# Performance work log

Measured on AMD Instinct MI355X. Metric: run time of the kernel, lower is better.

The kernel has to match this reference:

```python
import jax, jax.numpy as jnp
import numpy as np

INPUT_SIZE = 500
SENTENCE_SIZE = 128


def setup_inputs() -> dict:
    key = jax.random.key(0)
    ks = jax.random.split(key, 20)
    B, D = 16, 512
    Ho, Hi, Hu = 4, 4, 4
    dh_ori = D // Ho          # 128
    dh = D // (Hi + Hu)       # 64
    s = 0.05
    code = jax.random.normal(ks[0], (B, INPUT_SIZE, D), jnp.float32)
    # binary sentence-membership mask (which code tokens belong to each sentence)
    input_sentence = (jax.random.uniform(ks[1], (B, SENTENCE_SIZE, INPUT_SIZE)) < 0.2).astype(jnp.float32)

    def W(k, h, dout):
        return jax.random.normal(k, (h, D, dout), jnp.float32) * s

    def b(k, h, dout):
        return jax.random.normal(k, (h, dout), jnp.float32) * 0.01

    return dict(
        code=code, input_sentence=input_sentence,
        Wq_ori=W(ks[2], Ho, dh_ori), bq_ori=b(ks[3], Ho, dh_ori),
        Wk_ori=W(ks[4], Ho, dh_ori), bk_ori=b(ks[5], Ho, dh_ori),
        Wq_in=W(ks[6], Hi, dh), bq_in=b(ks[7], Hi, dh),
        Wk_in=W(ks[8], Hi, dh), bk_in=b(ks[9], Hi, dh),
        Wv_in=W(ks[10], Hi, dh), bv_in=b(ks[11], Hi, dh),
        Wq_out=W(ks[12], Hu, dh), bq_out=b(ks[13], Hu, dh),
        Wk_out=W(ks[14], Hu, dh), bk_out=b(ks[15], Hu, dh),
        Wv_out=W(ks[16], Hu, dh), bv_out=b(ks[17], Hu, dh),
    )


def _proj(x, W, b):
    # x: (B, N, D), W: (H, D, F), b: (H, F) -> (B, H, N, F), relu Dense per head
    return jax.nn.relu(jnp.einsum('bnd,hdf->bhnf', x, W) + b[:, None, :])


def reference(code, input_sentence,
              Wq_ori, bq_ori, Wk_ori, bk_ori,
              Wq_in, bq_in, Wk_in, bk_in, Wv_in, bv_in,
              Wq_out, bq_out, Wk_out, bk_out, Wv_out, bv_out):
    B, S = input_sentence.shape[0], input_sentence.shape[1]
    sent = input_sentence

    # ---- original (ori) branch: max over heads of raw QK^T, mask, matmul code ----
    q = _proj(code, Wq_ori, bq_ori)
    k = _proj(code, Wk_ori, bk_ori)
    scores_ori = jnp.einsum('bhnf,bhmf->bhnm', q, k).max(axis=1)      # (B, N, N)
    sA = jnp.einsum('bsn,bnm->bsm', sent, scores_ori)                 # (B, S, N)
    out_ori = jnp.einsum('bsm,bmd->bsd', sent * sA, code)             # (B, S, D)

    # ---- in-mask heads ----
    qi = _proj(code, Wq_in, bq_in)
    ki = _proj(code, Wk_in, bk_in)
    vi = _proj(code, Wv_in, bv_in)
    sc = jnp.einsum('bhnf,bhmf->bhnm', qi, ki)                        # (B, Hi, N, N)
    sAi = jnp.einsum('bsn,bhnm->bhsm', sent, sc)                      # (B, Hi, S, N)
    out_in = jnp.einsum('bhsm,bhmf->bhsf', sent[:, None] * sAi, vi)   # (B, Hi, S, F)

    # ---- out-mask heads ----
    qo = _proj(code, Wq_out, bq_out)
    ko = _proj(code, Wk_out, bk_out)
    vo = _proj(code, Wv_out, bv_out)
    sco = jnp.einsum('bhnf,bhmf->bhnm', qo, ko)
    sAo = jnp.einsum('bsn,bhnm->bhsm', sent, sco)
    masked = (sent - 1.0)[:, None] * sAo                              # (B, Hu, S, N)
    include = sent.sum(axis=2)[:, None, :, None]                      # (B, 1, S, 1)
    masked = masked / (INPUT_SIZE - include) * include
    out_out = jnp.einsum('bhsm,bhmf->bhsf', masked, vo)               # (B, Hu, S, F)

    # original returns a list [ori, in_0..in_Hi-1, out_0..out_Hu-1]; concat along features
    in_flat = jnp.transpose(out_in, (0, 2, 1, 3)).reshape(B, S, -1)
    out_flat = jnp.transpose(out_out, (0, 2, 1, 3)).reshape(B, S, -1)
    return jnp.concatenate([out_ori, in_flat, out_flat], axis=-1)
```

## Files before the change

kernel.cpp:

```cpp
#include <hip/hip_runtime.h>
#include <cfloat>

#define B_  16
#define N_  500
#define NP  512
#define S_  128
#define D_  512
#define FO  128
#define FI  64

typedef unsigned short u16;
typedef __attribute__((ext_vector_type(8))) short bf8;
typedef __attribute__((ext_vector_type(4))) float f4;

#define MFMA(a,b,c) __builtin_amdgcn_mfma_f32_16x16x32_bf16((a),(b),(c),0,0,0)

__device__ __forceinline__ u16 f2b(float x){
    union{float f;unsigned u;} v; v.f=x;
    unsigned r = v.u + 0x7fffu + ((v.u>>16)&1u);
    return (u16)(r>>16);
}
__device__ __forceinline__ float b2f(u16 x){
    union{unsigned u;float f;} v; v.u=((unsigned)x)<<16; return v.f;
}
__device__ __forceinline__ bf8 ldb8(const u16* p){ return *(const bf8*)p; }

__device__ __forceinline__ void gl2lds16(const u16* g, u16* lds){
    __builtin_amdgcn_global_load_lds(
        (const __attribute__((address_space(1))) unsigned int*)g,
        (__attribute__((address_space(3))) unsigned int*)lds, 16, 0, 0);
}

struct PWAll { const float* W[8]; u16* WT[8]; };
__global__ __launch_bounds__(256) void prep_fused(const float* __restrict__ code,
                                                  u16* __restrict__ codeB,
                                                  u16* __restrict__ codeT,
                                                  PWAll a,
                                                  const float* __restrict__ sent,
                                                  u16* __restrict__ sentB,
                                                  float* __restrict__ inc,
                                                  u16* a0, u16* a1, u16* a2, u16* a3)
{
    __shared__ float T[64][65];
    const int t = threadIdx.x;
    const int x = blockIdx.x;
    if (x < 1024){
        const int b  = x >> 6;
        const int m0 = ((x >> 3) & 7) * 64;
        const int d0 = (x & 7) * 64;
        #pragma unroll
        for (int i=0;i<16;++i){
            int idx = t + i*256; int rr = idx>>6, cc = idx&63;
            int m = m0+rr;
            T[rr][cc] = (m < N_) ? code[((size_t)b*N_+m)*D_ + d0+cc] : 0.f;
        }
        __syncthreads();
        #pragma unroll
        for (int i=0;i<16;++i){
            int idx=t+i*256; int rr=idx>>6, cc=idx&63; int m=m0+rr;
            if (m<N_) codeB[((size_t)b*N_+m)*D_ + d0+cc] = f2b(T[rr][cc]);
        }
        #pragma unroll
        for (int i=0;i<16;++i){
            int idx=t+i*256; int dd=idx>>6, mm=idx&63;
            codeT[((size_t)b*D_ + d0+dd)*NP + m0+mm] = f2b(T[mm][dd]);
        }
    } else if (x < 1344){
        const int v    = x - 1024;
        const int h    = v / 80;
        const int rem  = v - h*80;
        const int slot = rem >> 3;
        const int d0   = (rem & 7) * 64;
        const int widx = slot<4 ? (slot>>1) : slot-2;
        const int ftile= slot<4 ? (slot&1)  : 0;
        const int F    = slot<4 ? 128 : 64;
        const float* W = a.W[widx];
        u16* WT        = a.WT[widx];
        const int f0 = ftile*64;
        #pragma unroll
        for (int i=0;i<16;++i){
            int idx=t+i*256; int rr=idx>>6, cc=idx&63;
            T[rr][cc] = W[((size_t)h*D_ + d0+rr)*F + f0+cc];
        }
        __syncthreads();
        #pragma unroll
        for (int i=0;i<16;++i){
            int idx=t+i*256; int ff=idx>>6, dd=idx&63;
            WT[((size_t)h*F + f0+ff)*D_ + d0+dd] = f2b(T[dd][ff]);
        }
    } else if (x < 2368){
        const int y  = x - 1344;
        const int b  = y >> 6;
        const int s  = (y & 63)*2 + (t >> 7);
        const int tl = t & 127;
        const float* row = sent + ((size_t)b*S_+s)*N_;
        float4 v = make_float4(0.f,0.f,0.f,0.f);
        const int n = tl*4;
        if (n < N_) v = *(const float4*)(row+n);
        float sum = v.x+v.y+v.z+v.w;
        ushort4 o; o.x=f2b(v.x); o.y=f2b(v.y); o.z=f2b(v.z); o.w=f2b(v.w);
        *(ushort4*)&sentB[((size_t)b*S_+s)*NP + n] = o;
        #pragma unroll
        for (int off=32; off; off>>=1) sum += __shfl_down(sum, off);
        __shared__ float ls[4];
        if ((t&63)==0) ls[t>>6]=sum;
        __syncthreads();
        if (tl==0) inc[b*S_+s] = ls[(t>>7)*2] + ls[(t>>7)*2+1];
    } else {
        const int u  = x - 2368;
        u16* arr4[4] = {a0,a1,a2,a3};
        u16* base = arr4[u>>6] + (size_t)(u&63)*FI*NP;
        for (int idx=t; idx<FI*12; idx+=256){
            int f = idx/12, n = N_ + idx%12;
            base[(size_t)f*NP + n] = 0;
        }
    }
}

struct GemmOut { const float* bias[8]; u16* dst[8]; };
union ProjLDS {
    u16 ab[6][4096];
    u16 ot[16896];
};

#define PG_WAIT(NN) asm volatile("s_waitcnt vmcnt(" #NN ")" ::: "memory")
#define PG_FENCE()  asm volatile("" ::: "memory")

#define PG_STAGE(ai, bi, kk) { \
    gl2lds16(codeB + (size_t)(r0 + w*32      + srow)*D_ + (kk) + cgs, &L.ab[ai][(w*32)*32]);     \
    gl2lds16(WallT + (size_t)(c0 + w*32      + srow)*D_ + (kk) + cgs, &L.ab[bi][(w*32)*32]);     \
    gl2lds16(codeB + (size_t)(r0 + w*32 + 16 + srow)*D_ + (kk) + cgs, &L.ab[ai][(w*32+16)*32]);  \
    gl2lds16(WallT + (size_t)(c0 + w*32 + 16 + srow)*D_ + (kk) + cgs, &L.ab[bi][(w*32+16)*32]);  \
}

#define PG_COMPUTE(ai, bi) { \
    bf8 af[4], bfr[4]; \
    _Pragma("unroll") \
    for (int i=0;i<4;++i){ \
        af[i]  = *(const bf8*)&L.ab[ai][(wr + i*16 + lane16)*32 + kread]; \
        bfr[i] = *(const bf8*)&L.ab[bi][(wc + i*16 + lane16)*32 + kread]; \
    } \
    _Pragma("unroll") \
    for (int i=0;i<4;++i) \
        _Pragma("unroll") \
        for (int j=0;j<4;++j) \
            acc[i][j] = MFMA(af[i], bfr[j], acc[i][j]); \
}

#define PG_STEP(WN, ai, bi, jn) { \
    PG_WAIT(WN); \
    __builtin_amdgcn_s_barrier(); \
    PG_FENCE(); \
    __builtin_amdgcn_s_setprio(1); \
    PG_COMPUTE(ai, bi); \
    __builtin_amdgcn_s_setprio(0); \
    __builtin_amdgcn_s_barrier(); \
    PG_FENCE(); \
    if ((jn) < 16) PG_STAGE(ai, bi, (jn)*32); \
}

__global__ __launch_bounds__(256) void proj_gemm(const u16* __restrict__ codeB,
                                                 const u16* __restrict__ WallT,
                                                 GemmOut go)
{
    __shared__ alignas(16) ProjLDS L;

    const int t = threadIdx.x;
    const int w = t>>6, l = t&63, lane16 = l&15, lq = l>>4;
    const int bid = blockIdx.x;
    const int xcd = bid & 7;
    const int g   = bid >> 3;
    const int rt  = xcd*8 + g/20;
    const int ct  = g - (g/20)*20;
    const int r0 = rt*128;
    const int c0 = ct*128;
    const int wr = (w>>1)*64, wc = (w&1)*64;
    const int srow = l>>2;
    const int cgs  = ((l&3) ^ ((srow>>1)&3))*8;
    const int kread= (lq ^ ((lane16>>1)&3))*8;

    f4 acc[4][4] = {};

    PG_STAGE(0,3, 0);
    PG_STAGE(1,4, 32);
    PG_STAGE(2,5, 64);

    PG_STEP(8, 0,3, 3);
    PG_STEP(8, 1,4, 4);
    PG_STEP(8, 2,5, 5);
    PG_STEP(8, 0,3, 6);
    PG_STEP(8, 1,4, 7);
    PG_STEP(8, 2,5, 8);
    PG_STEP(8, 0,3, 9);
    PG_STEP(8, 1,4, 10);
    PG_STEP(8, 2,5, 11);
    PG_STEP(8, 0,3, 12);
    PG_STEP(8, 1,4, 13);
    PG_STEP(8, 2,5, 14);
    PG_STEP(8, 0,3, 15);
    PG_STEP(8, 1,4, 16);
    PG_STEP(4, 2,5, 17);
    PG_STEP(0, 0,3, 18);

    const int ri = (ct<4) ? 0 : (ct<8) ? 1 : 2 + ((ct-8)>>1);
    const bool tr = (ri==2)||(ri==4)||(ri==5)||(ri==7);

    __syncthreads();

    #pragma unroll
    for (int j=0;j<4;++j){
        const int c = c0 + wc + j*16 + lane16;
        const int idx = (c < 1024) ? (c & 511) : ((c-1024) & 255);
        const float bv = go.bias[ri][idx];
        if (tr){
            #pragma unroll
            for (int i=0;i<4;++i){
                ushort4 o4;
                float x0=acc[i][j][0]+bv, x1=acc[i][j][1]+bv, x2=acc[i][j][2]+bv, x3=acc[i][j][3]+bv;
                o4.x=f2b(x0>0.f?x0:0.f); o4.y=f2b(x1>0.f?x1:0.f);
                o4.z=f2b(x2>0.f?x2:0.f); o4.w=f2b(x3>0.f?x3:0.f);
                *(ushort4*)&L.ot[(wc+j*16+lane16)*132 + wr+i*16+lq*4] = o4;
            }
        } else {
            #pragma unroll
            for (int i=0;i<4;++i)
                #pragma unroll
                for (int reg=0;reg<4;++reg){
                    float x = acc[i][j][reg] + bv;
                    L.ot[(wr+i*16+lq*4+reg)*132 + wc+j*16+lane16] = f2b(x>0.f?x:0.f);
                }
        }
    }
    __syncthreads();

    if (tr){
        const int c  = t>>1;
        const int cg = c0 + c;
        const int u  = cg - 1024;
        const int hfv = u & 255, h = hfv>>6, f2 = hfv & 63;
        u16* dbase = go.dst[ri];
        const int half = t & 1;
        #pragma unroll
        for (int k2=0;k2<16;++k2){
            const int r  = half*64 + k2*4;
            const int rb = r0 + r;
            if (rb < 8000){
                const int b = rb/500, n = rb - b*500;
                *(ushort4*)&dbase[((size_t)(b*4+h)*FI + f2)*NP + n] =
                    *(const ushort4*)&L.ot[c*132 + r];
            }
        }
    } else {
        const int r  = t>>1;
        const int rb = r0 + r;
        if (rb < 8000){
            const int b = rb/500, n = rb - b*500;
            const int half = t & 1;
            const int cg0 = c0 + half*64;
            int h, f2base, F2;
            if (cg0 < 1024){ const int hf0 = cg0 & 511; h = hf0>>7; f2base = hf0 & 127; F2 = 128; }
            else           { const int hf0 = (cg0-1024) & 255; h = hf0>>6; f2base = hf0 & 63; F2 = 64; }
            u16* dstp = go.dst[ri] + ((size_t)(b*4+h)*N_ + n)*F2 + f2base;
            #pragma unroll
            for (int k2=0;k2<16;++k2)
                *(ushort4*)&dstp[k2*4] = *(const ushort4*)&L.ot[r*132 + half*64 + k2*4];
        }
    }
}

struct AttnArgs { const u16* qT[2]; const u16* kp[2]; const u16* vT[2]; };
struct MsLDS  { u16 Qs[64][136]; u16 Ks[128][136]; };
struct AtLDS  { float red[4][32][68]; u16 qsS[32][72]; u16 Pw[4][32][72]; };
union MALDS   { MsLDS ms; AtLDS at; };

__global__ __launch_bounds__(256) void msattn(const u16* __restrict__ q,
                                              const u16* __restrict__ k,
                                              u16* __restrict__ maxscT,
                                              AttnArgs a,
                                              const u16* __restrict__ sentB,
                                              const float* __restrict__ inc,
                                              float* __restrict__ out)
{
    __shared__ alignas(16) MALDS L;
    const int t=threadIdx.x, w=t>>6, l=t&63, lane16=l&15, lq=l>>4;
    const int idx = blockIdx.x >> 1;

    if ((blockIdx.x & 1) == 0){
        const int b=idx&15, n0=((idx>>4)&7)*64, m0=(idx>>7)*128;
        const int wr=(w>>1)*32, wc=(w&1)*64;

        f4 best[2][4];
        #pragma unroll
        for(int rt=0;rt<2;++rt)
            #pragma unroll
            for(int ct=0;ct<4;++ct)
                #pragma unroll
                for(int i=0;i<4;++i) best[rt][ct][i] = -FLT_MAX;

        for (int h=0;h<4;++h){
            const u16* qh = q + (size_t)(b*4+h)*N_*FO;
            const u16* kh = k + (size_t)(b*4+h)*N_*FO;
            #pragma unroll
            for (int i=0;i<4;++i){
                const int e=t+i*256, row=e>>4, kc=(e&15)*8;
                int n=n0+row; if(n>N_-1)n=N_-1;
                *(bf8*)&L.ms.Qs[row][kc] = ldb8(qh + (size_t)n*FO + kc);
            }
            #pragma unroll
            for (int i=0;i<8;++i){
                const int e=t+i*256, row=e>>4, kc=(e&15)*8;
                int m=m0+row; if(m>N_-1)m=N_-1;
                *(bf8*)&L.ms.Ks[row][kc] = ldb8(kh + (size_t)m*FO + kc);
            }
            __syncthreads();
            f4 acc[2][4]={};
            #pragma unroll
            for (int kk=0;kk<FO;kk+=32){
                bf8 a0=*(const bf8*)&L.ms.Qs[wr+lane16][kk+lq*8];
                bf8 a1=*(const bf8*)&L.ms.Qs[wr+16+lane16][kk+lq*8];
                #pragma unroll
                for(int ct=0;ct<4;++ct){
                    bf8 bb=*(const bf8*)&L.ms.Ks[wc+ct*16+lane16][kk+lq*8];
                    acc[0][ct]=MFMA(a0,bb,acc[0][ct]);
                    acc[1][ct]=MFMA(a1,bb,acc[1][ct]);
                }
            }
            #pragma unroll
            for(int rt=0;rt<2;++rt)
                #pragma unroll
                for(int ct=0;ct<4;++ct)
                    #pragma unroll
                    for(int i=0;i<4;++i) best[rt][ct][i] = fmaxf(best[rt][ct][i], acc[rt][ct][i]);
            __syncthreads();
        }
        #pragma unroll
        for(int rt=0;rt<2;++rt)
            #pragma unroll
            for(int ct=0;ct<4;++ct){
                const int m  = m0+wc+ct*16+lane16;
                const int nb = n0+wr+rt*16+lq*4;
                ushort4 o; o.x=f2b(best[rt][ct][0]); o.y=f2b(best[rt][ct][1]);
                o.z=f2b(best[rt][ct][2]); o.w=f2b(best[rt][ct][3]);
                *(ushort4*)&maxscT[((size_t)b*NP+m)*NP + nb] = o;
            }
    } else {
        const int bh=idx&63, b=bh>>2, h=bh&3, s0=((idx>>6)&3)*32, br=idx>>8;
        const u16* qT = a.qT[br];
        const u16* kp = a.kp[br];
        const u16* vT = a.vT[br];

        {
            const u16 *ap[2], *bp[4];
            #pragma unroll
            for(int rt=0;rt<2;++rt) ap[rt] = sentB + ((size_t)b*S_ + s0+rt*16+lane16)*NP + w*128 + lq*8;
            #pragma unroll
            for(int ct=0;ct<4;++ct) bp[ct] = qT + ((size_t)bh*FI + ct*16+lane16)*NP + w*128 + lq*8;
            f4 acc[2][4] = {};
            #pragma unroll
            for (int k0=0;k0<128;k0+=32){
                bf8 a0=ldb8(ap[0]+k0), a1=ldb8(ap[1]+k0);
                #pragma unroll
                for(int ct=0;ct<4;++ct){
                    bf8 bb=ldb8(bp[ct]+k0);
                    acc[0][ct]=MFMA(a0,bb,acc[0][ct]);
                    acc[1][ct]=MFMA(a1,bb,acc[1][ct]);
                }
            }
            #pragma unroll
            for(int rt=0;rt<2;++rt)
                #pragma unroll
                for(int ct=0;ct<4;++ct)
                    #pragma unroll
                    for(int reg=0;reg<4;++reg)
                        L.at.red[w][rt*16+lq*4+reg][ct*16+lane16] = acc[rt][ct][reg];
        }
        __syncthreads();
        {
            const int s=t>>3, f0=(t&7)*8;
            #pragma unroll
            for (int j=0;j<8;++j){
                float v = L.at.red[0][s][f0+j]+L.at.red[1][s][f0+j]
                        + L.at.red[2][s][f0+j]+L.at.red[3][s][f0+j];
                L.at.qsS[s][f0+j] = f2b(v);
            }
        }
        __syncthreads();

        f4 accO[2][4] = {};
        #pragma unroll
        for (int c=0;c<2;++c){
            const int m0 = w*64 + c*256;
            f4 p[2][4] = {};
            const u16* bp[4];
            #pragma unroll
            for(int ct=0;ct<4;++ct){
                int m=m0+ct*16+lane16; if(m>N_-1)m=N_-1;
                bp[ct] = kp + ((size_t)bh*N_+m)*FI + lq*8;
            }
            #pragma unroll
            for (int kk=0; kk<FI; kk+=32){
                bf8 a0 = *(const bf8*)&L.at.qsS[lane16][kk+lq*8];
                bf8 a1 = *(const bf8*)&L.at.qsS[16+lane16][kk+lq*8];
                #pragma unroll
                for(int ct=0;ct<4;++ct){
                    bf8 bb=ldb8(bp[ct]+kk);
                    p[0][ct]=MFMA(a0,bb,p[0][ct]);
                    p[1][ct]=MFMA(a1,bb,p[1][ct]);
                }
            }
            #pragma unroll
            for(int rt=0;rt<2;++rt)
                #pragma unroll
                for(int ct=0;ct<4;++ct){
                    const int m = m0+ct*16+lane16;
                    #pragma unroll
                    for(int reg=0;reg<4;++reg){
                        const int s = s0+rt*16+lq*4+reg;
                        const float sv = b2f(sentB[((size_t)b*S_+s)*NP+m]);
                        const float wgt = br ? ((m<N_)? sv-1.f : 0.f) : sv;
                        L.at.Pw[w][rt*16+lq*4+reg][ct*16+lane16] = f2b(p[rt][ct][reg]*wgt);
                    }
                }
            #pragma unroll
            for (int kk2=0; kk2<64; kk2+=32){
                bf8 a2[2];
                #pragma unroll
                for(int rt=0;rt<2;++rt) a2[rt] = *(const bf8*)&L.at.Pw[w][rt*16+lane16][kk2+lq*8];
                #pragma unroll
                for(int ct=0;ct<4;++ct){
                    bf8 vv = ldb8(vT + ((size_t)bh*FI + ct*16+lane16)*NP + m0+kk2+lq*8);
                    accO[0][ct]=MFMA(a2[0],vv,accO[0][ct]);
                    accO[1][ct]=MFMA(a2[1],vv,accO[1][ct]);
                }
            }
        }
        #pragma unroll
        for(int rt=0;rt<2;++rt)
            #pragma unroll
            for(int ct=0;ct<4;++ct)
                #pragma unroll
                for(int reg=0;reg<4;++reg)
                    L.at.red[w][rt*16+lq*4+reg][ct*16+lane16] = accO[rt][ct][reg];
        __syncthreads();
        {
            const int s=t>>3, f0=(t&7)*8;
            float fac = 1.f;
            if (br){ const float ic = inc[b*S_+s0+s]; fac = ic/(500.f-ic); }
            const size_t o = ((size_t)b*S_+s0+s)*1024 + (br?768:512) + h*FI + f0;
            #pragma unroll
            for (int j=0;j<8;++j){
                float v = L.at.red[0][s][f0+j]+L.at.red[1][s][f0+j]
                        + L.at.red[2][s][f0+j]+L.at.red[3][s][f0+j];
                out[o+j] = v*fac;
            }
        }
    }
}

__global__ __launch_bounds__(512) void saoo(const u16* __restrict__ sentB,
                                            const u16* __restrict__ maxscT,
                                            const u16* __restrict__ codeT,
                                            float* __restrict__ out)
{
    __shared__ u16 sAmS[16][520];
    const int b=blockIdx.x, s0=blockIdx.y*16;
    const int t=threadIdx.x, w=t>>6, l=t&63, lane16=l&15, lq=l>>4;

    {
        const int m0 = w*64;
        const u16* ap = sentB + ((size_t)b*S_ + s0+lane16)*NP + lq*8;
        const u16* bp[4];
        #pragma unroll
        for(int ct=0;ct<4;++ct) bp[ct] = maxscT + ((size_t)b*NP + m0+ct*16+lane16)*NP + lq*8;
        f4 acc[4] = {};
        for (int k0=0;k0<NP;k0+=32){
            bf8 av=ldb8(ap+k0);
            #pragma unroll
            for(int ct=0;ct<4;++ct) acc[ct]=MFMA(av, ldb8(bp[ct]+k0), acc[ct]);
        }
        #pragma unroll
        for(int ct=0;ct<4;++ct){
            const int m = m0+ct*16+lane16;
            #pragma unroll
            for(int reg=0;reg<4;++reg){
                const int s = s0+lq*4+reg;
                const float sv = b2f(sentB[((size_t)b*S_+s)*NP+m]);
                sAmS[lq*4+reg][m] = (sv != 0.f) ? f2b(acc[ct][reg]*sv) : (u16)0;
            }
        }
    }
    __syncthreads();
    {
        const int d0 = w*64;
        const u16* bp[4];
        #pragma unroll
        for(int ct=0;ct<4;++ct) bp[ct] = codeT + ((size_t)b*D_ + d0+ct*16+lane16)*NP + lq*8;
        f4 acc[4] = {};
        for (int k0=0;k0<NP;k0+=32){
            bf8 av = *(const bf8*)&sAmS[lane16][k0+lq*8];
            #pragma unroll
            for(int ct=0;ct<4;++ct) acc[ct]=MFMA(av, ldb8(bp[ct]+k0), acc[ct]);
        }
        #pragma unroll
        for(int ct=0;ct<4;++ct){
            const int d = d0+ct*16+lane16;
            #pragma unroll
            for(int reg=0;reg<4;++reg){
                const int s = s0+lq*4+reg;
                out[((size_t)b*S_+s)*1024 + d] = acc[ct][reg];
            }
        }
    }
}

extern "C" void kernel_launch(void* const* d_in, const int* in_sizes, int n_in,
                              void* d_out, int out_size, void* d_ws, size_t ws_size,
                              hipStream_t stream)
{
    const float* code   = (const float*)d_in[0];
    const float* sent   = (const float*)d_in[1];
    const float* Wq_ori = (const float*)d_in[2];
    const float* bq_ori = (const float*)d_in[3];
    const float* Wk_ori = (const float*)d_in[4];
    const float* bk_ori = (const float*)d_in[5];
    const float* Wq_in  = (const float*)d_in[6];
    const float* bq_in  = (const float*)d_in[7];
    const float* Wk_in  = (const float*)d_in[8];
    const float* bk_in  = (const float*)d_in[9];
    const float* Wv_in  = (const float*)d_in[10];
    const float* bv_in  = (const float*)d_in[11];
    const float* Wq_out = (const float*)d_in[12];
    const float* bq_out = (const float*)d_in[13];
    const float* Wk_out = (const float*)d_in[14];
    const float* bk_out = (const float*)d_in[15];
    const float* Wv_out = (const float*)d_in[16];
    const float* bv_out = (const float*)d_in[17];
    float* out = (float*)d_out;

    char* w = (char*)d_ws;
    u16*   codeB  = (u16*)(w);
    u16*   WallT  = (u16*)(w + 8388608);
    u16*   WTqo   = WallT;
    u16*   WTko   = WallT +  262144;
    u16*   WTqi   = WallT +  524288;
    u16*   WTki   = WallT +  655360;
    u16*   WTvi   = WallT +  786432;
    u16*   WTqu   = WallT +  917504;
    u16*   WTku   = WallT + 1048576;
    u16*   WTvu   = WallT + 1179648;
    u16*   sentB  = (u16*)(w + 11010048);
    float* incp   = (float*)(w + 13107200);
    u16* q_ori  = (u16*)(w + 13115392);
    u16* k_ori  = (u16*)(w + 21307392);
    u16* maxscT = (u16*)(w + 29499392);
    u16* codeT  = (u16*)(w + 37888000);
    u16* k_in   = (u16*)(w + 46276608);
    u16* k_out  = (u16*)(w + 50372608);
    u16* qT_in  = (u16*)(w + 54468608);
    u16* qT_out = (u16*)(w + 58662912);
    u16* vT_in  = (u16*)(w + 62857216);
    u16* vT_out = (u16*)(w + 67051520);

    PWAll pw;
    pw.W[0]=Wq_ori; pw.W[1]=Wk_ori; pw.W[2]=Wq_in; pw.W[3]=Wk_in;
    pw.W[4]=Wv_in;  pw.W[5]=Wq_out; pw.W[6]=Wk_out; pw.W[7]=Wv_out;
    pw.WT[0]=WTqo; pw.WT[1]=WTko; pw.WT[2]=WTqi; pw.WT[3]=WTki;
    pw.WT[4]=WTvi; pw.WT[5]=WTqu; pw.WT[6]=WTku; pw.WT[7]=WTvu;
    prep_fused<<<dim3(2624), 256, 0, stream>>>(code, codeB, codeT, pw,
                                               sent, sentB, incp,
                                               qT_in, qT_out, vT_in, vT_out);

    GemmOut go;
    go.bias[0]=bq_ori; go.bias[1]=bk_ori; go.bias[2]=bq_in; go.bias[3]=bk_in;
    go.bias[4]=bv_in;  go.bias[5]=bq_out; go.bias[6]=bk_out; go.bias[7]=bv_out;
    go.dst[0]=q_ori; go.dst[1]=k_ori; go.dst[2]=qT_in; go.dst[3]=k_in;
    go.dst[4]=vT_in; go.dst[5]=qT_out; go.dst[6]=k_out; go.dst[7]=vT_out;
    proj_gemm<<<dim3(1280), 256, 0, stream>>>(codeB, WallT, go);

    AttnArgs aa;
    aa.qT[0]=qT_in;  aa.qT[1]=qT_out;
    aa.kp[0]=k_in;   aa.kp[1]=k_out;
    aa.vT[0]=vT_in;  aa.vT[1]=vT_out;
    msattn<<<dim3(1024), 256, 0, stream>>>(q_ori, k_ori, maxscT, aa, sentB, incp, out);

    saoo<<<dim3(16,8), 512, 0, stream>>>(sentB, maxscT, codeT, out);
}
```

Measured before the change: 124.2 us.

## Rebalance kernel boundaries to overlap max-score attention with remaining projections

The projection GEMM is split in two. The first launch computes only the q_ori/k_ori columns. The second launch computes the remaining projection column tiles and, in the same grid, the max-over-heads score blocks that depend only on q_ori/k_ori. The per-head attention and the sentence/code matmul (saoo) are merged into one launch, with saoo blocks using 256 threads that each loop over two chunks. The aim is fewer serialized launches and better CU fill by co-scheduling independent work, at the cost of an extra launch and a larger shared-memory union.

```diff
diff --git a/kernel.cpp b/kernel.cpp
--- a/kernel.cpp
+++ b/kernel.cpp
@@ -127,18 +127,18 @@
 #define PG_FENCE()  asm volatile("" ::: "memory")
 
 #define PG_STAGE(ai, bi, kk) { \
-    gl2lds16(codeB + (size_t)(r0 + w*32      + srow)*D_ + (kk) + cgs, &L.ab[ai][(w*32)*32]);     \
-    gl2lds16(WallT + (size_t)(c0 + w*32      + srow)*D_ + (kk) + cgs, &L.ab[bi][(w*32)*32]);     \
-    gl2lds16(codeB + (size_t)(r0 + w*32 + 16 + srow)*D_ + (kk) + cgs, &L.ab[ai][(w*32+16)*32]);  \
-    gl2lds16(WallT + (size_t)(c0 + w*32 + 16 + srow)*D_ + (kk) + cgs, &L.ab[bi][(w*32+16)*32]);  \
+    gl2lds16(codeB + (size_t)(r0 + w*32      + srow)*D_ + (kk) + cgs, &Lp->ab[ai][(w*32)*32]);     \
+    gl2lds16(WallT + (size_t)(c0 + w*32      + srow)*D_ + (kk) + cgs, &Lp->ab[bi][(w*32)*32]);     \
+    gl2lds16(codeB + (size_t)(r0 + w*32 + 16 + srow)*D_ + (kk) + cgs, &Lp->ab[ai][(w*32+16)*32]);  \
+    gl2lds16(WallT + (size_t)(c0 + w*32 + 16 + srow)*D_ + (kk) + cgs, &Lp->ab[bi][(w*32+16)*32]);  \
 }
 
 #define PG_COMPUTE(ai, bi) { \
     bf8 af[4], bfr[4]; \
     _Pragma("unroll") \
     for (int i=0;i<4;++i){ \
-        af[i]  = *(const bf8*)&L.ab[ai][(wr + i*16 + lane16)*32 + kread]; \
-        bfr[i] = *(const bf8*)&L.ab[bi][(wc + i*16 + lane16)*32 + kread]; \
+        af[i]  = *(const bf8*)&Lp->ab[ai][(wr + i*16 + lane16)*32 + kread]; \
+        bfr[i] = *(const bf8*)&Lp->ab[bi][(wc + i*16 + lane16)*32 + kread]; \
     } \
     _Pragma("unroll") \
     for (int i=0;i<4;++i) \
@@ -159,19 +159,17 @@
     if ((jn) < 16) PG_STAGE(ai, bi, (jn)*32); \
 }
 
-__global__ __launch_bounds__(256) void proj_gemm(const u16* __restrict__ codeB,
+static __device__ __forceinline__ void proj_body(const u16* __restrict__ codeB,
                                                  const u16* __restrict__ WallT,
-                                                 GemmOut go)
+                                                 const GemmOut& go,
+                                                 ProjLDS* Lp,
+                                                 int bid, int t, int NCT, int CT0)
 {
-    __shared__ alignas(16) ProjLDS L;
-
-    const int t = threadIdx.x;
     const int w = t>>6, l = t&63, lane16 = l&15, lq = l>>4;
-    const int bid = blockIdx.x;
     const int xcd = bid & 7;
     const int g   = bid >> 3;
-    const int rt  = xcd*8 + g/20;
-    const int ct  = g - (g/20)*20;
+    const int rt  = xcd*8 + g/NCT;
+    const int ct  = CT0 + (g - (g/NCT)*NCT);
     const int r0 = rt*128;
     const int c0 = ct*128;
     const int wr = (w>>1)*64, wc = (w&1)*64;
@@ -219,7 +217,7 @@
                 float x0=acc[i][j][0]+bv, x1=acc[i][j][1]+bv, x2=acc[i][j][2]+bv, x3=acc[i][j][3]+bv;
                 o4.x=f2b(x0>0.f?x0:0.f); o4.y=f2b(x1>0.f?x1:0.f);
                 o4.z=f2b(x2>0.f?x2:0.f); o4.w=f2b(x3>0.f?x3:0.f);
-                *(ushort4*)&L.ot[(wc+j*16+lane16)*132 + wr+i*16+lq*4] = o4;
+                *(ushort4*)&Lp->ot[(wc+j*16+lane16)*132 + wr+i*16+lq*4] = o4;
             }
         } else {
             #pragma unroll
@@ -227,7 +225,7 @@
                 #pragma unroll
                 for (int reg=0;reg<4;++reg){
                     float x = acc[i][j][reg] + bv;
-                    L.ot[(wr+i*16+lq*4+reg)*132 + wc+j*16+lane16] = f2b(x>0.f?x:0.f);
+                    Lp->ot[(wr+i*16+lq*4+reg)*132 + wc+j*16+lane16] = f2b(x>0.f?x:0.f);
                 }
         }
     }
@@ -247,7 +245,7 @@
             if (rb < 8000){
                 const int b = rb/500, n = rb - b*500;
                 *(ushort4*)&dbase[((size_t)(b*4+h)*FI + f2)*NP + n] =
-                    *(const ushort4*)&L.ot[c*132 + r];
+                    *(const ushort4*)&Lp->ot[c*132 + r];
             }
         }
     } else {
@@ -263,88 +261,113 @@
             u16* dstp = go.dst[ri] + ((size_t)(b*4+h)*N_ + n)*F2 + f2base;
             #pragma unroll
             for (int k2=0;k2<16;++k2)
-                *(ushort4*)&dstp[k2*4] = *(const ushort4*)&L.ot[r*132 + half*64 + k2*4];
+                *(ushort4*)&dstp[k2*4] = *(const ushort4*)&Lp->ot[r*132 + half*64 + k2*4];
         }
     }
 }
 
+__global__ __launch_bounds__(256) void proj_a(const u16* __restrict__ codeB,
+                                              const u16* __restrict__ WallT,
+                                              GemmOut go)
+{
+    __shared__ alignas(16) ProjLDS L;
+    proj_body(codeB, WallT, go, &L, blockIdx.x, threadIdx.x, 8, 0);
+}
+
+struct MsLDS  { u16 Qs[64][136]; u16 Ks[128][136]; };
+union PMLDS   { ProjLDS p; MsLDS ms; };
+
+__global__ __launch_bounds__(256) void projfi_ms(const u16* __restrict__ codeB,
+                                                 const u16* __restrict__ WallT,
+                                                 GemmOut go,
+                                                 const u16* __restrict__ q,
+                                                 const u16* __restrict__ k,
+                                                 u16* __restrict__ maxscT)
+{
+    __shared__ alignas(16) PMLDS L;
+    const int t=threadIdx.x, x=blockIdx.x;
+    if (x < 768){
+        proj_body(codeB, WallT, go, &L.p, x, t, 12, 8);
+        return;
+    }
+    const int idx = x - 768;
+    const int w=t>>6, l=t&63, lane16=l&15, lq=l>>4;
+    const int b=idx&15, n0=((idx>>4)&7)*64, m0=(idx>>7)*128;
+    const int wr=(w>>1)*32, wc=(w&1)*64;
+
+    f4 best[2][4];
+    #pragma unroll
+    for(int rt=0;rt<2;++rt)
+        #pragma unroll
+        for(int ct=0;ct<4;++ct)
+            #pragma unroll
+            for(int i=0;i<4;++i) best[rt][ct][i] = -FLT_MAX;
+
+    for (int h=0;h<4;++h){
+        const u16* qh = q + (size_t)(b*4+h)*N_*FO;
+        const u16* kh = k + (size_t)(b*4+h)*N_*FO;
+        #pragma unroll
+        for (int i=0;i<4;++i){
+            const int e=t+i*256, row=e>>4, kc=(e&15)*8;
+            int n=n0+row; if(n>N_-1)n=N_-1;
+            *(bf8*)&L.ms.Qs[row][kc] = ldb8(qh + (size_t)n*FO + kc);
+        }
+        #pragma unroll
+        for (int i=0;i<8;++i){
+            const int e=t+i*256, row=e>>4, kc=(e&15)*8;
+            int m=m0+row; if(m>N_-1)m=N_-1;
+            *(bf8*)&L.ms.Ks[row][kc] = ldb8(kh + (size_t)m*FO + kc);
+        }
+        __syncthreads();
+        f4 acc[2][4]={};
+        #pragma unroll
+        for (int kk=0;kk<FO;kk+=32){
+            bf8 a0=*(const bf8*)&L.ms.Qs[wr+lane16][kk+lq*8];
+            bf8 a1=*(const bf8*)&L.ms.Qs[wr+16+lane16][kk+lq*8];
+            #pragma unroll
+            for(int ct=0;ct<4;++ct){
+                bf8 bb=*(const bf8*)&L.ms.Ks[wc+ct*16+lane16][kk+lq*8];
+                acc[0][ct]=MFMA(a0,bb,acc[0][ct]);
+                acc[1][ct]=MFMA(a1,bb,acc[1][ct]);
+            }
+        }
+        #pragma unroll
+        for(int rt=0;rt<2;++rt)
+            #pragma unroll
+            for(int ct=0;ct<4;++ct)
+                #pragma unroll
+                for(int i=0;i<4;++i) best[rt][ct][i] = fmaxf(best[rt][ct][i], acc[rt][ct][i]);
+        __syncthreads();
+    }
+    #pragma unroll
+    for(int rt=0;rt<2;++rt)
+        #pragma unroll
+        for(int ct=0;ct<4;++ct){
+            const int m  = m0+wc+ct*16+lane16;
+            const int nb = n0+wr+rt*16+lq*4;
+            ushort4 o; o.x=f2b(best[rt][ct][0]); o.y=f2b(best[rt][ct][1]);
+            o.z=f2b(best[rt][ct][2]); o.w=f2b(best[rt][ct][3]);
+            *(ushort4*)&maxscT[((size_t)b*NP+m)*NP + nb] = o;
+        }
+}
+
 struct AttnArgs { const u16* qT[2]; const u16* kp[2]; const u16* vT[2]; };
-struct MsLDS  { u16 Qs[64][136]; u16 Ks[128][136]; };
 struct AtLDS  { float red[4][32][68]; u16 qsS[32][72]; u16 Pw[4][32][72]; };
-union MALDS   { MsLDS ms; AtLDS at; };
-
-__global__ __launch_bounds__(256) void msattn(const u16* __restrict__ q,
-                                              const u16* __restrict__ k,
-                                              u16* __restrict__ maxscT,
-                                              AttnArgs a,
-                                              const u16* __restrict__ sentB,
-                                              const float* __restrict__ inc,
-                                              float* __restrict__ out)
+union ASLDS   { AtLDS at; u16 sAmS[16][520]; };
+
+__global__ __launch_bounds__(256) void attn_saoo(AttnArgs a,
+                                                 const u16* __restrict__ sentB,
+                                                 const float* __restrict__ inc,
+                                                 const u16* __restrict__ maxscT,
+                                                 const u16* __restrict__ codeT,
+                                                 float* __restrict__ out)
 {
-    __shared__ alignas(16) MALDS L;
+    __shared__ alignas(16) ASLDS L;
     const int t=threadIdx.x, w=t>>6, l=t&63, lane16=l&15, lq=l>>4;
-    const int idx = blockIdx.x >> 1;
-
-    if ((blockIdx.x & 1) == 0){
-        const int b=idx&15, n0=((idx>>4)&7)*64, m0=(idx>>7)*128;
-        const int wr=(w>>1)*32, wc=(w&1)*64;
-
-        f4 best[2][4];
-        #pragma unroll
-        for(int rt=0;rt<2;++rt)
-            #pragma unroll
-            for(int ct=0;ct<4;++ct)
-                #pragma unroll
-                for(int i=0;i<4;++i) best[rt][ct][i] = -FLT_MAX;
-
-        for (int h=0;h<4;++h){
-            const u16* qh = q + (size_t)(b*4+h)*N_*FO;
-            const u16* kh = k + (size_t)(b*4+h)*N_*FO;
-            #pragma unroll
-            for (int i=0;i<4;++i){
-                const int e=t+i*256, row=e>>4, kc=(e&15)*8;
-                int n=n0+row; if(n>N_-1)n=N_-1;
-                *(bf8*)&L.ms.Qs[row][kc] = ldb8(qh + (size_t)n*FO + kc);
-            }
-            #pragma unroll
-            for (int i=0;i<8;++i){
-                const int e=t+i*256, row=e>>4, kc=(e&15)*8;
-                int m=m0+row; if(m>N_-1)m=N_-1;
-                *(bf8*)&L.ms.Ks[row][kc] = ldb8(kh + (size_t)m*FO + kc);
-            }
-            __syncthreads();
-            f4 acc[2][4]={};
-            #pragma unroll
-            for (int kk=0;kk<FO;kk+=32){
-                bf8 a0=*(const bf8*)&L.ms.Qs[wr+lane16][kk+lq*8];
-                bf8 a1=*(const bf8*)&L.ms.Qs[wr+16+lane16][kk+lq*8];
-                #pragma unroll
-                for(int ct=0;ct<4;++ct){
-                    bf8 bb=*(const bf8*)&L.ms.Ks[wc+ct*16+lane16][kk+lq*8];
-                    acc[0][ct]=MFMA(a0,bb,acc[0][ct]);
-                    acc[1][ct]=MFMA(a1,bb,acc[1][ct]);
-                }
-            }
-            #pragma unroll
-            for(int rt=0;rt<2;++rt)
-                #pragma unroll
-                for(int ct=0;ct<4;++ct)
-                    #pragma unroll
-                    for(int i=0;i<4;++i) best[rt][ct][i] = fmaxf(best[rt][ct][i], acc[rt][ct][i]);
-            __syncthreads();
-        }
-        #pragma unroll
-        for(int rt=0;rt<2;++rt)
-            #pragma unroll
-            for(int ct=0;ct<4;++ct){
-                const int m  = m0+wc+ct*16+lane16;
-                const int nb = n0+wr+rt*16+lq*4;
-                ushort4 o; o.x=f2b(best[rt][ct][0]); o.y=f2b(best[rt][ct][1]);
-                o.z=f2b(best[rt][ct][2]); o.w=f2b(best[rt][ct][3]);
-                *(ushort4*)&maxscT[((size_t)b*NP+m)*NP + nb] = o;
-            }
-    } else {
-        const int bh=idx&63, b=bh>>2, h=bh&3, s0=((idx>>6)&3)*32, br=idx>>8;
+    const int x = blockIdx.x;
+
+    if (x < 512){
+        const int idx=x, bh=idx&63, b=bh>>2, h=bh&3, s0=((idx>>6)&3)*32, br=idx>>8;
         const u16* qT = a.qT[br];
         const u16* kp = a.kp[br];
         const u16* vT = a.vT[br];
@@ -454,60 +477,55 @@
                 out[o+j] = v*fac;
             }
         }
-    }
-}
-
-__global__ __launch_bounds__(512) void saoo(const u16* __restrict__ sentB,
-                                            const u16* __restrict__ maxscT,
-                                            const u16* __restrict__ codeT,
-                                            float* __restrict__ out)
-{
-    __shared__ u16 sAmS[16][520];
-    const int b=blockIdx.x, s0=blockIdx.y*16;
-    const int t=threadIdx.x, w=t>>6, l=t&63, lane16=l&15, lq=l>>4;
-
-    {
-        const int m0 = w*64;
-        const u16* ap = sentB + ((size_t)b*S_ + s0+lane16)*NP + lq*8;
-        const u16* bp[4];
-        #pragma unroll
-        for(int ct=0;ct<4;++ct) bp[ct] = maxscT + ((size_t)b*NP + m0+ct*16+lane16)*NP + lq*8;
-        f4 acc[4] = {};
-        for (int k0=0;k0<NP;k0+=32){
-            bf8 av=ldb8(ap+k0);
-            #pragma unroll
-            for(int ct=0;ct<4;++ct) acc[ct]=MFMA(av, ldb8(bp[ct]+k0), acc[ct]);
-        }
-        #pragma unroll
-        for(int ct=0;ct<4;++ct){
-            const int m = m0+ct*16+lane16;
-            #pragma unroll
-            for(int reg=0;reg<4;++reg){
-                const int s = s0+lq*4+reg;
-                const float sv = b2f(sentB[((size_t)b*S_+s)*NP+m]);
-                sAmS[lq*4+reg][m] = (sv != 0.f) ? f2b(acc[ct][reg]*sv) : (u16)0;
-            }
-        }
-    }
-    __syncthreads();
-    {
-        const int d0 = w*64;
-        const u16* bp[4];
-        #pragma unroll
-        for(int ct=0;ct<4;++ct) bp[ct] = codeT + ((size_t)b*D_ + d0+ct*16+lane16)*NP + lq*8;
-        f4 acc[4] = {};
-        for (int k0=0;k0<NP;k0+=32){
-            bf8 av = *(const bf8*)&sAmS[lane16][k0+lq*8];
-            #pragma unroll
-            for(int ct=0;ct<4;++ct) acc[ct]=MFMA(av, ldb8(bp[ct]+k0), acc[ct]);
-        }
-        #pragma unroll
-        for(int ct=0;ct<4;++ct){
-            const int d = d0+ct*16+lane16;
-            #pragma unroll
-            for(int reg=0;reg<4;++reg){
-                const int s = s0+lq*4+reg;
-                out[((size_t)b*S_+s)*1024 + d] = acc[ct][reg];
+    } else {
+        const int idx = x - 512;
+        const int b = idx>>3, s0 = (idx&7)*16;
+
+        #pragma unroll
+        for (int c=0;c<2;++c){
+            const int m0 = (w + c*4)*64;
+            const u16* ap = sentB + ((size_t)b*S_ + s0+lane16)*NP + lq*8;
+            const u16* bp[4];
+            #pragma unroll
+            for(int ct=0;ct<4;++ct) bp[ct] = maxscT + ((size_t)b*NP + m0+ct*16+lane16)*NP + lq*8;
+            f4 acc[4] = {};
+            for (int k0=0;k0<NP;k0+=32){
+                bf8 av=ldb8(ap+k0);
+                #pragma unroll
+                for(int ct=0;ct<4;++ct) acc[ct]=MFMA(av, ldb8(bp[ct]+k0), acc[ct]);
+            }
+            #pragma unroll
+            for(int ct=0;ct<4;++ct){
+                const int m = m0+ct*16+lane16;
+                #pragma unroll
+                for(int reg=0;reg<4;++reg){
+                    const int s = s0+lq*4+reg;
+                    const float sv = b2f(sentB[((size_t)b*S_+s)*NP+m]);
+                    L.sAmS[lq*4+reg][m] = (sv != 0.f) ? f2b(acc[ct][reg]*sv) : (u16)0;
+                }
+            }
+        }
+        __syncthreads();
+        #pragma unroll
+        for (int c=0;c<2;++c){
+            const int d0 = (w + c*4)*64;
+            const u16* bp[4];
+            #pragma unroll
+            for(int ct=0;ct<4;++ct) bp[ct] = codeT + ((size_t)b*D_ + d0+ct*16+lane16)*NP + lq*8;
+            f4 acc[4] = {};
+            for (int k0=0;k0<NP;k0+=32){
+                bf8 av = *(const bf8*)&L.sAmS[lane16][k0+lq*8];
+                #pragma unroll
+                for(int ct=0;ct<4;++ct) acc[ct]=MFMA(av, ldb8(bp[ct]+k0), acc[ct]);
+            }
+            #pragma unroll
+            for(int ct=0;ct<4;++ct){
+                const int d = d0+ct*16+lane16;
+                #pragma unroll
+                for(int reg=0;reg<4;++reg){
+                    const int s = s0+lq*4+reg;
+                    out[((size_t)b*S_+s)*1024 + d] = acc[ct][reg];
+                }
             }
         }
     }
@@ -575,13 +593,14 @@
     go.bias[4]=bv_in;  go.bias[5]=bq_out; go.bias[6]=bk_out; go.bias[7]=bv_out;
     go.dst[0]=q_ori; go.dst[1]=k_ori; go.dst[2]=qT_in; go.dst[3]=k_in;
     go.dst[4]=vT_in; go.dst[5]=qT_out; go.dst[6]=k_out; go.dst[7]=vT_out;
-    proj_gemm<<<dim3(1280), 256, 0, stream>>>(codeB, WallT, go);
+
+    proj_a<<<dim3(512), 256, 0, stream>>>(codeB, WallT, go);
+
+    projfi_ms<<<dim3(1280), 256, 0, stream>>>(codeB, WallT, go, q_ori, k_ori, maxscT);
 
     AttnArgs aa;
     aa.qT[0]=qT_in;  aa.qT[1]=qT_out;
     aa.kp[0]=k_in;   aa.kp[1]=k_out;
     aa.vT[0]=vT_in;  aa.vT[1]=vT_out;
-    msattn<<<dim3(1024), 256, 0, stream>>>(q_ori, k_ori, maxscT, aa, sentB, incp, out);
-
-    saoo<<<dim3(16,8), 512, 0, stream>>>(sentB, maxscT, codeT, out);
-}
+    attn_saoo<<<dim3(640), 256, 0, stream>>>(aa, sentB, incp, maxscT, codeT, out);
+}
```

Result: slower. 129.4 us (+4.2%).
